# Kernel tuning notes

Measured on AMD Instinct MI355X. Metric: run time of the kernel, lower is better.

Reference implementation:

```python
import jax, jax.numpy as jnp
import numpy as np


def setup_inputs() -> dict:
    key = jax.random.key(0)
    k1, k2, k3, k4 = jax.random.split(key, 4)
    B, T, E, H = 8, 2048, 1024, 64
    x = jax.random.normal(k1, (B, T, E), dtype=jnp.float32)
    # scale params like typical init to keep logits sane
    Wk = jax.random.normal(k2, (E, H), dtype=jnp.float32) * (E ** -0.5)
    Wq = jax.random.normal(k3, (E, H), dtype=jnp.float32) * (E ** -0.5)
    Wv = jax.random.normal(k4, (E, H), dtype=jnp.float32) * (E ** -0.5)
    return {"x": x, "Wk": Wk, "Wq": Wq, "Wv": Wv}


def reference(x, Wk, Wq, Wv):
    # x: [B, T, E]; Wk/Wq/Wv: [E, H]
    T = x.shape[1]
    H = Wk.shape[1]
    k = jnp.einsum('bte,eh->bth', x, Wk)
    q = jnp.einsum('bte,eh->bth', x, Wq)
    v = jnp.einsum('bte,eh->bth', x, Wv)
    # scaled scores [B, T, T]
    wei = jnp.einsum('bqh,bkh->bqk', q, k) * (H ** -0.5)
    causal = jnp.tril(jnp.ones((T, T), dtype=bool))  # tril buffer
    wei = jnp.where(causal, wei, -jnp.inf)
    wei = jax.nn.softmax(wei, axis=-1)
    # dropout p=0.0 (eval): identity
    return jnp.einsum('bqk,bkh->bqh', wei, v)
```

## Files before the change

### kernel.cpp

```cpp
#include <hip/hip_runtime.h>
#include <math.h>

constexpr int B_ = 8, T_ = 2048, E_ = 1024, H_ = 64;
constexpr long BT = (long)B_ * T_;

typedef __attribute__((ext_vector_type(8))) short bf16x8;
typedef __attribute__((ext_vector_type(4))) float f32x4;

__device__ inline unsigned short bf16_rne(float f) {
    union { float f; unsigned u; } v; v.f = f;
    unsigned u = v.u + (0x7FFFu + ((v.u >> 16) & 1u));
    return (unsigned short)(u >> 16);
}
__device__ inline unsigned pack_bf16x2(float lo, float hi) {
    return (unsigned)bf16_rne(lo) | ((unsigned)bf16_rne(hi) << 16);
}

__device__ inline void load_lds16(const void* g, void* l) {
    __builtin_amdgcn_global_load_lds(
        (const __attribute__((address_space(1))) void*)(uintptr_t)g,
        (__attribute__((address_space(3))) void*)(unsigned)(uintptr_t)l,
        16, 0, 0);
}

constexpr float QS = 0.18033688011112042f;

__global__ __launch_bounds__(256) void wt_build_k(
    const float* __restrict__ Wk, const float* __restrict__ Wq,
    const float* __restrict__ Wv, unsigned short* __restrict__ Wt)
{
    const int d    = blockIdx.x * 256 + threadIdx.x;
    const int tile = d >> 6;
    const int lq   = d & 63;
    const int quad = lq >> 4;
    const int l16  = lq & 15;
    const int kc   = tile / 12;
    const int nt   = tile - kc * 12;
    const int n    = nt * 16 + l16;

    const float* src; int col; float s = 1.0f;
    if (n < 64)       { src = Wk; col = n; }
    else if (n < 128) { src = Wq; col = n - 64; s = QS; }
    else              { src = Wv; col = n - 128; }

    const int kk0 = kc * 32 + quad * 8;
    const float* sp = src + (size_t)kk0 * H_ + col;
    unsigned p[4];
    #pragma unroll
    for (int jj = 0; jj < 4; jj++)
        p[jj] = pack_bf16x2(sp[(2 * jj) * H_] * s, sp[(2 * jj + 1) * H_] * s);
    *(uint4*)(Wt + (size_t)d * 8) = make_uint4(p[0], p[1], p[2], p[3]);
}

__global__ __launch_bounds__(512, 4) void qkv_mfma_k(
    const float* __restrict__ x, const unsigned short* __restrict__ Wt,
    unsigned short* __restrict__ kO, unsigned short* __restrict__ qO,
    unsigned short* __restrict__ vfO)
{
    __shared__ float4 xs[2][32][16];
    __shared__ unsigned short VL[32][66];

    const int t    = threadIdx.x;
    const int w    = t >> 6;
    const int l    = t & 63;
    const int l16  = l & 15;
    const int quad = l >> 4;
    const int rg   = w >> 2;
    const int nq   = w & 3;
    const int row0 = blockIdx.x * 32 + rg * 16;
    const int row0b = blockIdx.x * 32;

    const int rr = w * 4 + (l >> 4);
    const int cc = l & 15;
    const int gg = cc ^ (rr & 7);
    const float* gsrc = x + (size_t)(row0b + rr) * E_ + gg * 4;

    const int r  = rg * 16 + l16;
    const int rx = r & 7;

    f32x4 acc[3];
    #pragma unroll
    for (int n = 0; n < 3; n++) acc[n] = (f32x4){0.f, 0.f, 0.f, 0.f};

    load_lds16(gsrc, &xs[0][rr][cc]);

    for (int it = 0; it < 16; ++it) {
        const int buf = it & 1;
        __syncthreads();
        if (it + 1 < 16)
            load_lds16(gsrc + (it + 1) * 64, &xs[buf ^ 1][rr][cc]);

        #pragma unroll
        for (int kk = 0; kk < 2; ++kk) {
            const int G0 = kk * 8 + quad * 2;
            float4 fa = xs[buf][r][G0 ^ rx];
            float4 fb = xs[buf][r][(G0 + 1) ^ rx];

            const int kc = it * 2 + kk;
            const unsigned short* wpp = Wt + (size_t)(kc * 12 + nq * 3) * 512 + (size_t)l * 8;
            bf16x8 b0 = *(const bf16x8*)(wpp);
            bf16x8 b1 = *(const bf16x8*)(wpp + 512);
            bf16x8 b2 = *(const bf16x8*)(wpp + 1024);

            union { bf16x8 v; unsigned u[4]; } av;
            av.u[0] = pack_bf16x2(fa.x, fa.y);
            av.u[1] = pack_bf16x2(fa.z, fa.w);
            av.u[2] = pack_bf16x2(fb.x, fb.y);
            av.u[3] = pack_bf16x2(fb.z, fb.w);

            acc[0] = __builtin_amdgcn_mfma_f32_16x16x32_bf16(av.v, b0, acc[0], 0, 0, 0);
            acc[1] = __builtin_amdgcn_mfma_f32_16x16x32_bf16(av.v, b1, acc[1], 0, 0, 0);
            acc[2] = __builtin_amdgcn_mfma_f32_16x16x32_bf16(av.v, b2, acc[2], 0, 0, 0);
        }
    }

    #pragma unroll
    for (int n = 0; n < 3; n++) {
        const int gn = nq * 3 + n;
        const int hb = gn * 16 + l16;
        if (gn < 4) {
            #pragma unroll
            for (int rr2 = 0; rr2 < 4; rr2++) {
                const int row = row0 + quad * 4 + rr2;
                kO[(size_t)row * H_ + hb] = bf16_rne(acc[n][rr2]);
            }
        } else if (gn < 8) {
            #pragma unroll
            for (int rr2 = 0; rr2 < 4; rr2++) {
                const int row = row0 + quad * 4 + rr2;
                qO[(size_t)row * H_ + (hb - 64)] = bf16_rne(acc[n][rr2]);
            }
        } else {
            #pragma unroll
            for (int rr2 = 0; rr2 < 4; rr2++)
                VL[rg * 16 + quad * 4 + rr2][(gn - 8) * 16 + l16] = bf16_rne(acc[n][rr2]);
        }
    }
    __syncthreads();

    if (t < 256) {
        const int g  = t >> 6;
        const int lf = t & 15;
        const int qf = (t >> 4) & 3;
        unsigned pk[4];
        #pragma unroll
        for (int jj = 0; jj < 4; jj++) {
            const int p0 = qf * 8 + 2 * jj;
            const int i0 = (p0 >> 1) | ((p0 & 1) << 4);
            const int p1 = p0 + 1;
            const int i1 = (p1 >> 1) | ((p1 & 1) << 4);
            pk[jj] = (unsigned)VL[i0][g * 16 + lf]
                   | ((unsigned)VL[i1][g * 16 + lf] << 16);
        }
        const int tile = blockIdx.x;
        *(uint4*)(vfO + ((size_t)tile * 4 + g) * 512 + (size_t)(t & 63) * 8) =
            make_uint4(pk[0], pk[1], pk[2], pk[3]);
    }
}

__global__ __launch_bounds__(256, 4) void attn_mfma(
    const unsigned short* __restrict__ q,
    const unsigned short* __restrict__ k,
    const unsigned short* __restrict__ vf,
    float* __restrict__ out)
{
    __shared__ unsigned short Pl[4][16 * 40];
    __shared__ float Ot[4][16][68];
    __shared__ float lsW[4][16];

    const int t    = threadIdx.x;
    const int w    = t >> 6;
    const int l    = t & 63;
    const int l16  = l & 15;
    const int quad = l >> 4;

    const int b    = blockIdx.x & 7;
    const int qidx = blockIdx.x >> 3;
    const int qt   = (qidx & 1) ? (127 - (qidx >> 1)) : (qidx >> 1);
    const int t0   = qt * 16;
    const int nk   = t0 / 32 + 1;

    const size_t qoff = ((size_t)b * T_ + t0 + l16) * H_ + quad * 8;
    bf16x8 aq0 = *(const bf16x8*)(q + qoff);
    bf16x8 aq1 = *(const bf16x8*)(q + qoff + 32);

    f32x4 o[4];
    #pragma unroll
    for (int g = 0; g < 4; g++) o[g] = (f32x4){0.f, 0.f, 0.f, 0.f};
    float ls[4] = {0.f, 0.f, 0.f, 0.f};

    const unsigned short* kbp = k + (size_t)b * T_ * H_;
    const unsigned short* vbp = vf + (size_t)b * 64 * 2048 + (size_t)l * 8;
    unsigned short* Pw = &Pl[w][0];

    bf16x8 bk00, bk01, bk10, bk11, bv0, bv1, bv2, bv3;
    if (w < nk) {
        const int kbase = w * 32;
        const unsigned short* kp = kbp + (size_t)(kbase + l16) * H_ + quad * 8;
        bk00 = *(const bf16x8*)(kp);
        bk01 = *(const bf16x8*)(kp + 32);
        bk10 = *(const bf16x8*)(kp + 16 * H_);
        bk11 = *(const bf16x8*)(kp + 16 * H_ + 32);
        const unsigned short* vp = vbp + (size_t)w * 2048;
        bv0 = *(const bf16x8*)(vp);
        bv1 = *(const bf16x8*)(vp + 512);
        bv2 = *(const bf16x8*)(vp + 1024);
        bv3 = *(const bf16x8*)(vp + 1536);
    }

    for (int kt = w; kt < nk; kt += 4) {
        const int ktn    = (kt + 4 < nk) ? kt + 4 : kt;
        const int kbasen = ktn * 32;
        const unsigned short* kpn = kbp + (size_t)(kbasen + l16) * H_ + quad * 8;
        bf16x8 nk00 = *(const bf16x8*)(kpn);
        bf16x8 nk01 = *(const bf16x8*)(kpn + 32);
        bf16x8 nk10 = *(const bf16x8*)(kpn + 16 * H_);
        bf16x8 nk11 = *(const bf16x8*)(kpn + 16 * H_ + 32);
        const unsigned short* vpn = vbp + (size_t)ktn * 2048;
        bf16x8 nv0 = *(const bf16x8*)(vpn);
        bf16x8 nv1 = *(const bf16x8*)(vpn + 512);
        bf16x8 nv2 = *(const bf16x8*)(vpn + 1024);
        bf16x8 nv3 = *(const bf16x8*)(vpn + 1536);

        const int kbase = kt * 32;
        f32x4 s0 = (f32x4){0.f, 0.f, 0.f, 0.f};
        f32x4 s1 = (f32x4){0.f, 0.f, 0.f, 0.f};
        s0 = __builtin_amdgcn_mfma_f32_16x16x32_bf16(aq0, bk00, s0, 0, 0, 0);
        s0 = __builtin_amdgcn_mfma_f32_16x16x32_bf16(aq1, bk01, s0, 0, 0, 0);
        s1 = __builtin_amdgcn_mfma_f32_16x16x32_bf16(aq0, bk10, s1, 0, 0, 0);
        s1 = __builtin_amdgcn_mfma_f32_16x16x32_bf16(aq1, bk11, s1, 0, 0, 0);

        if (kbase + 31 > t0) {
            const int rowb = t0 + quad * 4;
            #pragma unroll
            for (int r = 0; r < 4; r++) {
                if (kbase + l16 > rowb + r)      s0[r] = -3.0e38f;
                if (kbase + 16 + l16 > rowb + r) s1[r] = -3.0e38f;
            }
        }

        #pragma unroll
        for (int r = 0; r < 4; r++) {
            float p0 = exp2f(s0[r]);
            float p1 = exp2f(s1[r]);
            ls[r] += p0 + p1;
            *(unsigned*)(Pw + (quad * 4 + r) * 40 + 2 * l16) = pack_bf16x2(p0, p1);
        }
        asm volatile("s_waitcnt lgkmcnt(0)" ::: "memory");
        bf16x8 ap = *(const bf16x8*)(Pw + l16 * 40 + quad * 8);

        o[0] = __builtin_amdgcn_mfma_f32_16x16x32_bf16(ap, bv0, o[0], 0, 0, 0);
        o[1] = __builtin_amdgcn_mfma_f32_16x16x32_bf16(ap, bv1, o[1], 0, 0, 0);
        o[2] = __builtin_amdgcn_mfma_f32_16x16x32_bf16(ap, bv2, o[2], 0, 0, 0);
        o[3] = __builtin_amdgcn_mfma_f32_16x16x32_bf16(ap, bv3, o[3], 0, 0, 0);

        bk00 = nk00; bk01 = nk01; bk10 = nk10; bk11 = nk11;
        bv0 = nv0; bv1 = nv1; bv2 = nv2; bv3 = nv3;
    }

    #pragma unroll
    for (int r = 0; r < 4; r++) {
        float s = ls[r];
        s += __shfl_xor(s, 1);
        s += __shfl_xor(s, 2);
        s += __shfl_xor(s, 4);
        s += __shfl_xor(s, 8);
        ls[r] = s;
    }
    if (l16 == 0) {
        #pragma unroll
        for (int r = 0; r < 4; r++) lsW[w][quad * 4 + r] = ls[r];
    }
    #pragma unroll
    for (int g = 0; g < 4; g++)
        #pragma unroll
        for (int r = 0; r < 4; r++)
            Ot[w][quad * 4 + r][g * 16 + l16] = o[g][r];
    __syncthreads();

    {
        const int col = w * 16 + l16;
        #pragma unroll
        for (int r = 0; r < 4; r++) {
            const int row = quad * 4 + r;
            float L  = lsW[0][row] + lsW[1][row] + lsW[2][row] + lsW[3][row];
            float sv = Ot[0][row][col] + Ot[1][row][col]
                     + Ot[2][row][col] + Ot[3][row][col];
            out[((size_t)b * T_ + t0 + row) * H_ + col] = sv / L;
        }
    }
}

extern "C" void kernel_launch(void* const* d_in, const int* in_sizes, int n_in,
                              void* d_out, int out_size, void* d_ws, size_t ws_size,
                              hipStream_t stream)
{
    const float* x  = (const float*)d_in[0];
    const float* Wk = (const float*)d_in[1];
    const float* Wq = (const float*)d_in[2];
    const float* Wv = (const float*)d_in[3];

    unsigned short* wt    = (unsigned short*)d_ws;
    unsigned short* kbuf  = wt + 24576 * 8;
    unsigned short* qbuf  = kbuf + BT * H_;
    unsigned short* vfbuf = qbuf + BT * H_;
    float* outp = (float*)d_out;

    wt_build_k<<<96, 256, 0, stream>>>(Wk, Wq, Wv, wt);
    qkv_mfma_k<<<(B_ * T_) / 32, 512, 0, stream>>>(x, wt, kbuf, qbuf, vfbuf);
    attn_mfma<<<B_ * 128, 256, 0, stream>>>(qbuf, kbuf, vfbuf, outp);
}
```

Measured before the change: 150.0 us.

## Double-buffer K/V tiles in LDS via direct global-to-LDS loads

```diff
diff --git a/kernel.cpp b/kernel.cpp
--- a/kernel.cpp
+++ b/kernel.cpp
@@ -158,15 +158,14 @@
     }
 }
 
-__global__ __launch_bounds__(256, 4) void attn_mfma(
+__global__ __launch_bounds__(256, 2) void attn_mfma(
     const unsigned short* __restrict__ q,
     const unsigned short* __restrict__ k,
     const unsigned short* __restrict__ vf,
     float* __restrict__ out)
 {
+    __shared__ __align__(16) unsigned short KV[4][2][4096];
     __shared__ unsigned short Pl[4][16 * 40];
-    __shared__ float Ot[4][16][68];
-    __shared__ float lsW[4][16];
 
     const int t    = threadIdx.x;
     const int w    = t >> 6;
@@ -189,38 +188,47 @@
     for (int g = 0; g < 4; g++) o[g] = (f32x4){0.f, 0.f, 0.f, 0.f};
     float ls[4] = {0.f, 0.f, 0.f, 0.f};
 
-    const unsigned short* kbp = k + (size_t)b * T_ * H_;
-    const unsigned short* vbp = vf + (size_t)b * 64 * 2048 + (size_t)l * 8;
+    const unsigned short* kbp = k  + (size_t)b * T_ * H_;
+    const unsigned short* vfb = vf + (size_t)b * 64 * 2048;
     unsigned short* Pw = &Pl[w][0];
-
-    bf16x8 bk00, bk01, bk10, bk11, bv0, bv1, bv2, bv3;
-    if (w < nk) {
-        const int kbase = w * 32;
+    unsigned short* kv0 = &KV[w][0][0];
+    unsigned short* kv1 = &KV[w][1][0];
+
+    auto issue_tile = [&](int kt, unsigned short* dst) {
+        const int kbase = kt * 32;
         const unsigned short* kp = kbp + (size_t)(kbase + l16) * H_ + quad * 8;
-        bk00 = *(const bf16x8*)(kp);
-        bk01 = *(const bf16x8*)(kp + 32);
-        bk10 = *(const bf16x8*)(kp + 16 * H_);
-        bk11 = *(const bf16x8*)(kp + 16 * H_ + 32);
-        const unsigned short* vp = vbp + (size_t)w * 2048;
-        bv0 = *(const bf16x8*)(vp);
-        bv1 = *(const bf16x8*)(vp + 512);
-        bv2 = *(const bf16x8*)(vp + 1024);
-        bv3 = *(const bf16x8*)(vp + 1536);
-    }
-
-    for (int kt = w; kt < nk; kt += 4) {
-        const int ktn    = (kt + 4 < nk) ? kt + 4 : kt;
-        const int kbasen = ktn * 32;
-        const unsigned short* kpn = kbp + (size_t)(kbasen + l16) * H_ + quad * 8;
-        bf16x8 nk00 = *(const bf16x8*)(kpn);
-        bf16x8 nk01 = *(const bf16x8*)(kpn + 32);
-        bf16x8 nk10 = *(const bf16x8*)(kpn + 16 * H_);
-        bf16x8 nk11 = *(const bf16x8*)(kpn + 16 * H_ + 32);
-        const unsigned short* vpn = vbp + (size_t)ktn * 2048;
-        bf16x8 nv0 = *(const bf16x8*)(vpn);
-        bf16x8 nv1 = *(const bf16x8*)(vpn + 512);
-        bf16x8 nv2 = *(const bf16x8*)(vpn + 1024);
-        bf16x8 nv3 = *(const bf16x8*)(vpn + 1536);
+        load_lds16(kp,               dst + 0 * 512 + l * 8);
+        load_lds16(kp + 32,          dst + 1 * 512 + l * 8);
+        load_lds16(kp + 16 * H_,     dst + 2 * 512 + l * 8);
+        load_lds16(kp + 16 * H_ + 32, dst + 3 * 512 + l * 8);
+        const unsigned short* vp = vfb + (size_t)kt * 2048 + l * 8;
+        load_lds16(vp,        dst + 4 * 512 + l * 8);
+        load_lds16(vp + 512,  dst + 5 * 512 + l * 8);
+        load_lds16(vp + 1024, dst + 6 * 512 + l * 8);
+        load_lds16(vp + 1536, dst + 7 * 512 + l * 8);
+    };
+
+    if (w < nk) issue_tile(w, kv0);
+
+    int it = 0;
+    for (int kt = w; kt < nk; kt += 4, ++it) {
+        unsigned short* cur = (it & 1) ? kv1 : kv0;
+        unsigned short* nxt = (it & 1) ? kv0 : kv1;
+        if (kt + 4 < nk) {
+            issue_tile(kt + 4, nxt);
+            asm volatile("s_waitcnt vmcnt(8)" ::: "memory");
+        } else {
+            asm volatile("s_waitcnt vmcnt(0)" ::: "memory");
+        }
+
+        bf16x8 bk00 = *(const bf16x8*)(cur + 0 * 512 + l * 8);
+        bf16x8 bk01 = *(const bf16x8*)(cur + 1 * 512 + l * 8);
+        bf16x8 bk10 = *(const bf16x8*)(cur + 2 * 512 + l * 8);
+        bf16x8 bk11 = *(const bf16x8*)(cur + 3 * 512 + l * 8);
+        bf16x8 bv0  = *(const bf16x8*)(cur + 4 * 512 + l * 8);
+        bf16x8 bv1  = *(const bf16x8*)(cur + 5 * 512 + l * 8);
+        bf16x8 bv2  = *(const bf16x8*)(cur + 6 * 512 + l * 8);
+        bf16x8 bv3  = *(const bf16x8*)(cur + 7 * 512 + l * 8);
 
         const int kbase = kt * 32;
         f32x4 s0 = (f32x4){0.f, 0.f, 0.f, 0.f};
@@ -253,9 +261,6 @@
         o[1] = __builtin_amdgcn_mfma_f32_16x16x32_bf16(ap, bv1, o[1], 0, 0, 0);
         o[2] = __builtin_amdgcn_mfma_f32_16x16x32_bf16(ap, bv2, o[2], 0, 0, 0);
         o[3] = __builtin_amdgcn_mfma_f32_16x16x32_bf16(ap, bv3, o[3], 0, 0, 0);
-
-        bk00 = nk00; bk01 = nk01; bk10 = nk10; bk11 = nk11;
-        bv0 = nv0; bv1 = nv1; bv2 = nv2; bv3 = nv3;
     }
 
     #pragma unroll
@@ -267,15 +272,19 @@
         s += __shfl_xor(s, 8);
         ls[r] = s;
     }
+
+    __syncthreads();
+    float* otb = (float*)&KV[0][0][0];
+    float* lsW = otb + 4 * 16 * 68;
     if (l16 == 0) {
         #pragma unroll
-        for (int r = 0; r < 4; r++) lsW[w][quad * 4 + r] = ls[r];
+        for (int r = 0; r < 4; r++) lsW[w * 16 + quad * 4 + r] = ls[r];
     }
     #pragma unroll
     for (int g = 0; g < 4; g++)
         #pragma unroll
         for (int r = 0; r < 4; r++)
-            Ot[w][quad * 4 + r][g * 16 + l16] = o[g][r];
+            otb[((w * 16) + quad * 4 + r) * 68 + g * 16 + l16] = o[g][r];
     __syncthreads();
 
     {
@@ -283,9 +292,10 @@
         #pragma unroll
         for (int r = 0; r < 4; r++) {
             const int row = quad * 4 + r;
-            float L  = lsW[0][row] + lsW[1][row] + lsW[2][row] + lsW[3][row];
-            float sv = Ot[0][row][col] + Ot[1][row][col]
-                     + Ot[2][row][col] + Ot[3][row][col];
+            float L  = lsW[0 * 16 + row] + lsW[1 * 16 + row]
+                     + lsW[2 * 16 + row] + lsW[3 * 16 + row];
+            float sv = otb[(0 * 16 + row) * 68 + col] + otb[(1 * 16 + row) * 68 + col]
+                     + otb[(2 * 16 + row) * 68 + col] + otb[(3 * 16 + row) * 68 + col];
             out[((size_t)b * T_ + t0 + row) * H_ + col] = sv / L;
         }
     }
```

New measurement: 148.3 us. Within noise of the previous version (-1.1%).

## Compute transposed scores to keep P in registers and hand-pipeline K/V loads

Applied to the files above, without the earlier changes.

```diff
diff --git a/kernel.cpp b/kernel.cpp
--- a/kernel.cpp
+++ b/kernel.cpp
@@ -21,6 +21,12 @@
         (const __attribute__((address_space(1))) void*)(uintptr_t)g,
         (__attribute__((address_space(3))) void*)(unsigned)(uintptr_t)l,
         16, 0, 0);
+}
+
+__device__ inline bf16x8 gload16(const unsigned short* p) {
+    bf16x8 r;
+    asm volatile("global_load_dwordx4 %0, %1, off" : "=v"(r) : "v"(p));
+    return r;
 }
 
 constexpr float QS = 0.18033688011112042f;
@@ -145,18 +151,74 @@
         unsigned pk[4];
         #pragma unroll
         for (int jj = 0; jj < 4; jj++) {
-            const int p0 = qf * 8 + 2 * jj;
-            const int i0 = (p0 >> 1) | ((p0 & 1) << 4);
-            const int p1 = p0 + 1;
-            const int i1 = (p1 >> 1) | ((p1 & 1) << 4);
-            pk[jj] = (unsigned)VL[i0][g * 16 + lf]
-                   | ((unsigned)VL[i1][g * 16 + lf] << 16);
+            const int jb   = 2 * jj;
+            const int key0 = (jb < 4) ? (qf * 4 + jb) : (16 + qf * 4 + (jb - 4));
+            const int key1 = key0 + 1;
+            pk[jj] = (unsigned)VL[key0][g * 16 + lf]
+                   | ((unsigned)VL[key1][g * 16 + lf] << 16);
         }
         const int tile = blockIdx.x;
         *(uint4*)(vfO + ((size_t)tile * 4 + g) * 512 + (size_t)(t & 63) * 8) =
             make_uint4(pk[0], pk[1], pk[2], pk[3]);
     }
 }
+
+#define ISSUE_K(kt, K0, K1, K2, K3) do {                                     \
+    const unsigned short* _kp = kbp + (size_t)((kt) * 32 + l16) * H_ + quad * 8; \
+    K0 = gload16(_kp);                                                       \
+    K1 = gload16(_kp + 32);                                                  \
+    K2 = gload16(_kp + 16 * H_);                                             \
+    K3 = gload16(_kp + 16 * H_ + 32);                                        \
+} while (0)
+
+#define ISSUE_V(kt) do {                                                     \
+    const unsigned short* _vp = vfb + (size_t)(kt) * 2048 + l * 8;           \
+    V0 = gload16(_vp);                                                       \
+    V1 = gload16(_vp + 512);                                                 \
+    V2 = gload16(_vp + 1024);                                                \
+    V3 = gload16(_vp + 1536);                                                \
+} while (0)
+
+#define WAITK(K0, K1, K2, K3)                                                \
+    asm volatile("s_waitcnt vmcnt(8)"                                        \
+        : "+v"(K0), "+v"(K1), "+v"(K2), "+v"(K3) : : "memory")
+
+#define WAITV()                                                              \
+    asm volatile("s_waitcnt vmcnt(4)"                                        \
+        : "+v"(V0), "+v"(V1), "+v"(V2), "+v"(V3) : : "memory")
+
+#define BODYQK(kb, K0, K1, K2, K3) do {                                      \
+    s0 = (f32x4){0.f, 0.f, 0.f, 0.f};                                        \
+    s1 = (f32x4){0.f, 0.f, 0.f, 0.f};                                        \
+    s0 = __builtin_amdgcn_mfma_f32_16x16x32_bf16(K0, aq0, s0, 0, 0, 0);      \
+    s0 = __builtin_amdgcn_mfma_f32_16x16x32_bf16(K1, aq1, s0, 0, 0, 0);      \
+    s1 = __builtin_amdgcn_mfma_f32_16x16x32_bf16(K2, aq0, s1, 0, 0, 0);      \
+    s1 = __builtin_amdgcn_mfma_f32_16x16x32_bf16(K3, aq1, s1, 0, 0, 0);      \
+    if ((kb) + 31 > t0) {                                                    \
+        const int qrow = t0 + l16;                                           \
+        _Pragma("unroll")                                                    \
+        for (int r = 0; r < 4; r++) {                                        \
+            if ((kb) + quad * 4 + r > qrow)      s0[r] = -3.0e38f;           \
+            if ((kb) + 16 + quad * 4 + r > qrow) s1[r] = -3.0e38f;           \
+        }                                                                    \
+    }                                                                        \
+    float p0[4], p1[4];                                                      \
+    _Pragma("unroll")                                                        \
+    for (int r = 0; r < 4; r++) { p0[r] = exp2f(s0[r]); p1[r] = exp2f(s1[r]); } \
+    lsp += (p0[0] + p0[1]) + (p0[2] + p0[3])                                 \
+         + (p1[0] + p1[1]) + (p1[2] + p1[3]);                                \
+    av.u[0] = pack_bf16x2(p0[0], p0[1]);                                     \
+    av.u[1] = pack_bf16x2(p0[2], p0[3]);                                     \
+    av.u[2] = pack_bf16x2(p1[0], p1[1]);                                     \
+    av.u[3] = pack_bf16x2(p1[2], p1[3]);                                     \
+} while (0)
+
+#define BODYPV() do {                                                        \
+    o[0] = __builtin_amdgcn_mfma_f32_16x16x32_bf16(av.v, V0, o[0], 0, 0, 0); \
+    o[1] = __builtin_amdgcn_mfma_f32_16x16x32_bf16(av.v, V1, o[1], 0, 0, 0); \
+    o[2] = __builtin_amdgcn_mfma_f32_16x16x32_bf16(av.v, V2, o[2], 0, 0, 0); \
+    o[3] = __builtin_amdgcn_mfma_f32_16x16x32_bf16(av.v, V3, o[3], 0, 0, 0); \
+} while (0)
 
 __global__ __launch_bounds__(256, 4) void attn_mfma(
     const unsigned short* __restrict__ q,
@@ -164,7 +226,6 @@
     const unsigned short* __restrict__ vf,
     float* __restrict__ out)
 {
-    __shared__ unsigned short Pl[4][16 * 40];
     __shared__ float Ot[4][16][68];
     __shared__ float lsW[4][16];
 
@@ -180,97 +241,53 @@
     const int t0   = qt * 16;
     const int nk   = t0 / 32 + 1;
 
-    const size_t qoff = ((size_t)b * T_ + t0 + l16) * H_ + quad * 8;
-    bf16x8 aq0 = *(const bf16x8*)(q + qoff);
-    bf16x8 aq1 = *(const bf16x8*)(q + qoff + 32);
+    const unsigned short* kbp = k  + (size_t)b * T_ * H_;
+    const unsigned short* vfb = vf + (size_t)b * 64 * 2048;
+
+    const unsigned short* qp = q + ((size_t)b * T_ + t0 + l16) * H_ + quad * 8;
+    bf16x8 aq0 = gload16(qp);
+    bf16x8 aq1 = gload16(qp + 32);
 
     f32x4 o[4];
     #pragma unroll
     for (int g = 0; g < 4; g++) o[g] = (f32x4){0.f, 0.f, 0.f, 0.f};
-    float ls[4] = {0.f, 0.f, 0.f, 0.f};
-
-    const unsigned short* kbp = k + (size_t)b * T_ * H_;
-    const unsigned short* vbp = vf + (size_t)b * 64 * 2048 + (size_t)l * 8;
-    unsigned short* Pw = &Pl[w][0];
-
-    bf16x8 bk00, bk01, bk10, bk11, bv0, bv1, bv2, bv3;
-    if (w < nk) {
-        const int kbase = w * 32;
-        const unsigned short* kp = kbp + (size_t)(kbase + l16) * H_ + quad * 8;
-        bk00 = *(const bf16x8*)(kp);
-        bk01 = *(const bf16x8*)(kp + 32);
-        bk10 = *(const bf16x8*)(kp + 16 * H_);
-        bk11 = *(const bf16x8*)(kp + 16 * H_ + 32);
-        const unsigned short* vp = vbp + (size_t)w * 2048;
-        bv0 = *(const bf16x8*)(vp);
-        bv1 = *(const bf16x8*)(vp + 512);
-        bv2 = *(const bf16x8*)(vp + 1024);
-        bv3 = *(const bf16x8*)(vp + 1536);
-    }
-
-    for (int kt = w; kt < nk; kt += 4) {
-        const int ktn    = (kt + 4 < nk) ? kt + 4 : kt;
-        const int kbasen = ktn * 32;
-        const unsigned short* kpn = kbp + (size_t)(kbasen + l16) * H_ + quad * 8;
-        bf16x8 nk00 = *(const bf16x8*)(kpn);
-        bf16x8 nk01 = *(const bf16x8*)(kpn + 32);
-        bf16x8 nk10 = *(const bf16x8*)(kpn + 16 * H_);
-        bf16x8 nk11 = *(const bf16x8*)(kpn + 16 * H_ + 32);
-        const unsigned short* vpn = vbp + (size_t)ktn * 2048;
-        bf16x8 nv0 = *(const bf16x8*)(vpn);
-        bf16x8 nv1 = *(const bf16x8*)(vpn + 512);
-        bf16x8 nv2 = *(const bf16x8*)(vpn + 1024);
-        bf16x8 nv3 = *(const bf16x8*)(vpn + 1536);
-
-        const int kbase = kt * 32;
-        f32x4 s0 = (f32x4){0.f, 0.f, 0.f, 0.f};
-        f32x4 s1 = (f32x4){0.f, 0.f, 0.f, 0.f};
-        s0 = __builtin_amdgcn_mfma_f32_16x16x32_bf16(aq0, bk00, s0, 0, 0, 0);
-        s0 = __builtin_amdgcn_mfma_f32_16x16x32_bf16(aq1, bk01, s0, 0, 0, 0);
-        s1 = __builtin_amdgcn_mfma_f32_16x16x32_bf16(aq0, bk10, s1, 0, 0, 0);
-        s1 = __builtin_amdgcn_mfma_f32_16x16x32_bf16(aq1, bk11, s1, 0, 0, 0);
-
-        if (kbase + 31 > t0) {
-            const int rowb = t0 + quad * 4;
-            #pragma unroll
-            for (int r = 0; r < 4; r++) {
-                if (kbase + l16 > rowb + r)      s0[r] = -3.0e38f;
-                if (kbase + 16 + l16 > rowb + r) s1[r] = -3.0e38f;
-            }
-        }
-
-        #pragma unroll
-        for (int r = 0; r < 4; r++) {
-            float p0 = exp2f(s0[r]);
-            float p1 = exp2f(s1[r]);
-            ls[r] += p0 + p1;
-            *(unsigned*)(Pw + (quad * 4 + r) * 40 + 2 * l16) = pack_bf16x2(p0, p1);
-        }
-        asm volatile("s_waitcnt lgkmcnt(0)" ::: "memory");
-        bf16x8 ap = *(const bf16x8*)(Pw + l16 * 40 + quad * 8);
-
-        o[0] = __builtin_amdgcn_mfma_f32_16x16x32_bf16(ap, bv0, o[0], 0, 0, 0);
-        o[1] = __builtin_amdgcn_mfma_f32_16x16x32_bf16(ap, bv1, o[1], 0, 0, 0);
-        o[2] = __builtin_amdgcn_mfma_f32_16x16x32_bf16(ap, bv2, o[2], 0, 0, 0);
-        o[3] = __builtin_amdgcn_mfma_f32_16x16x32_bf16(ap, bv3, o[3], 0, 0, 0);
-
-        bk00 = nk00; bk01 = nk01; bk10 = nk10; bk11 = nk11;
-        bv0 = nv0; bv1 = nv1; bv2 = nv2; bv3 = nv3;
-    }
-
-    #pragma unroll
-    for (int r = 0; r < 4; r++) {
-        float s = ls[r];
-        s += __shfl_xor(s, 1);
-        s += __shfl_xor(s, 2);
-        s += __shfl_xor(s, 4);
-        s += __shfl_xor(s, 8);
-        ls[r] = s;
-    }
-    if (l16 == 0) {
-        #pragma unroll
-        for (int r = 0; r < 4; r++) lsW[w][quad * 4 + r] = ls[r];
-    }
+    float lsp = 0.f;
+
+    bf16x8 A0, A1, A2, A3, B0, B1, B2, B3, V0, V1, V2, V3;
+    union { bf16x8 v; unsigned u[4]; } av;
+    f32x4 s0, s1;
+
+    int kt = w;
+    if (kt < nk) {
+        ISSUE_K(kt, A0, A1, A2, A3);
+        ISSUE_V(kt);
+        asm volatile("s_waitcnt vmcnt(8)" : "+v"(aq0), "+v"(aq1) : : "memory");
+        while (true) {
+            int kn = (kt + 4 < nk) ? kt + 4 : kt;
+            ISSUE_K(kn, B0, B1, B2, B3);
+            WAITK(A0, A1, A2, A3);
+            BODYQK(kt * 32, A0, A1, A2, A3);
+            WAITV();
+            BODYPV();
+            kt += 4; if (kt >= nk) break;
+            ISSUE_V(kt);
+
+            kn = (kt + 4 < nk) ? kt + 4 : kt;
+            ISSUE_K(kn, A0, A1, A2, A3);
+            WAITK(B0, B1, B2, B3);
+            BODYQK(kt * 32, B0, B1, B2, B3);
+            WAITV();
+            BODYPV();
+            kt += 4; if (kt >= nk) break;
+            ISSUE_V(kt);
+        }
+    }
+    asm volatile("s_waitcnt vmcnt(0)" ::: "memory");
+
+    lsp += __shfl_xor(lsp, 16);
+    lsp += __shfl_xor(lsp, 32);
+    if (l < 16) lsW[w][l] = lsp;
+
     #pragma unroll
     for (int g = 0; g < 4; g++)
         #pragma unroll
```

Result: no change. 149.9 us (-0.0%).
